# Kernel tuning notes

Hardware: AMD Instinct MI355X
Metric: run time of the kernel (lower is better)

Reference implementation:

```python
import jax, jax.numpy as jnp
import numpy as np

BLOCK_SPLIT = (4, 4, 4)
GRID = 256
N_BLOCK = 64
BX = GRID // 4  # 64, per-block grid resolution along each axis
N_PTS = 4_194_304


def setup_inputs() -> dict:
    key = jax.random.key(0)
    k1, k2 = jax.random.split(key)
    aabb = jnp.array([[-1.5, -1.5, -1.5], [1.5, 1.5, 1.5]], dtype=jnp.float32)
    # points roughly inside the aabb
    xyz_sampled = jax.random.uniform(k1, (N_PTS, 3), dtype=jnp.float32) * 3.0 - 1.5
    alpha_volume = jax.random.uniform(k2, (GRID, GRID, GRID), dtype=jnp.float32)
    # per-block domains (as kilonerf global_to_local expects): block AABBs
    idx = np.stack(np.meshgrid(np.arange(4), np.arange(4), np.arange(4), indexing='ij'), -1).reshape(-1, 3)
    voxel = np.array([3.0 / 4.0] * 3)
    dmin = (-1.5 + idx * voxel).astype(np.float32)
    dmax = (dmin + voxel).astype(np.float32)
    return {"xyz_sampled": xyz_sampled, "aabb": aabb, "alpha_volume": alpha_volume,
            "domain_min": jnp.asarray(dmin), "domain_max": jnp.asarray(dmax)}


def _sample_alpha(xyz, aabb, alpha_volume, dmin, dmax):
    bs = jnp.asarray(BLOCK_SPLIT, jnp.float32)
    voxel = (aabb[1] - aabb[0]) / bs                      # per-block world size
    idx3 = jnp.floor((xyz - aabb[0]) / voxel).astype(jnp.int32)
    idx3 = jnp.clip(idx3, 0, jnp.array(BLOCK_SPLIT, jnp.int32) - 1)  # edge clamp (matches loop)
    strides = jnp.array([BLOCK_SPLIT[2] * BLOCK_SPLIT[1], BLOCK_SPLIT[2], 1], jnp.int32)
    bid = (idx3 * strides).sum(-1)                        # [N] block id in [0, 64)

    order = jnp.argsort(bid)                              # jax sort is stable; matches bucket-by-block order
    bid_s = bid[order]
    pts = xyz[order]

    # global_to_local (kilonerf): map into per-block [-1,1]^3
    local = 2.0 * (pts - dmin[bid_s]) / (dmax[bid_s] - dmin[bid_s]) - 1.0  # [N,3] (gx,gy,gz)

    # torch .view(64,1,64,64,64) is a raw contiguous reinterpretation -> plain reshape
    vols = alpha_volume.reshape(N_BLOCK, BX, BX, BX)      # [B, D, H, W]
    D = H = W = BX
    # grid_sample convention: grid x -> W axis, y -> H axis, z -> D axis; align_corners=True
    fx = (local[:, 0] + 1.0) * 0.5 * (W - 1)
    fy = (local[:, 1] + 1.0) * 0.5 * (H - 1)
    fz = (local[:, 2] + 1.0) * 0.5 * (D - 1)
    x0 = jnp.floor(fx); y0 = jnp.floor(fy); z0 = jnp.floor(fz)
    wx = fx - x0; wy = fy - y0; wz = fz - z0
    x0i = x0.astype(jnp.int32); y0i = y0.astype(jnp.int32); z0i = z0.astype(jnp.int32)

    def fetch(zi, yi, xi):
        # zeros padding for out-of-range corners (grid_sample padding_mode='zeros')
        inb = (zi >= 0) & (zi < D) & (yi >= 0) & (yi < H) & (xi >= 0) & (xi < W)
        v = vols[bid_s, jnp.clip(zi, 0, D - 1), jnp.clip(yi, 0, H - 1), jnp.clip(xi, 0, W - 1)]
        return jnp.where(inb, v, 0.0)

    out = jnp.zeros_like(fx)
    for dz, wz_ in ((0, 1.0 - wz), (1, wz)):
        for dy, wy_ in ((0, 1.0 - wy), (1, wy)):
            for dx, wx_ in ((0, 1.0 - wx), (1, wx)):
                out = out + wz_ * wy_ * wx_ * fetch(z0i + dz, y0i + dy, x0i + dx)
    return out  # [N] alpha values in block-sorted order


def reference(xyz_sampled, aabb, alpha_volume, domain_min, domain_max):
    return _sample_alpha(xyz_sampled, aabb, alpha_volume, domain_min, domain_max)
```

## Files before the change

kernel.cpp:

```cpp
#include <hip/hip_runtime.h>

#define BLK    256
#define TILE_C 4096
#define NB     64
#define NF     4096
#define TILE_F 16384
#define FBLK   512

__device__ __forceinline__ int compute_bid(float px, float py, float pz,
                                           float a0x, float a0y, float a0z,
                                           float vx, float vy, float vz) {
    int ix = (int)floorf((px - a0x) / vx);
    int iy = (int)floorf((py - a0y) / vy);
    int iz = (int)floorf((pz - a0z) / vz);
    ix = min(max(ix, 0), 3);
    iy = min(max(iy, 0), 3);
    iz = min(max(iz, 0), 3);
    return ix * 16 + iy * 4 + iz;
}

__global__ void hist_kernel(const float* __restrict__ xyz,
                            const float* __restrict__ aabb,
                            int* __restrict__ hist, int N, int G) {
    __shared__ int s_h[NB];
    const int tid = threadIdx.x, g = blockIdx.x;
    if (tid < NB) s_h[tid] = 0;
    __syncthreads();
    const float a0x = aabb[0], a0y = aabb[1], a0z = aabb[2];
    const float vx = (aabb[3] - a0x) * 0.25f;
    const float vy = (aabb[4] - a0y) * 0.25f;
    const float vz = (aabb[5] - a0z) * 0.25f;
    for (int c = 0; c < TILE_C / (BLK * 4); ++c) {
        int p0 = g * TILE_C + c * (BLK * 4) + tid * 4;
        if (p0 + 3 < N) {
            const float4* v4 = (const float4*)(xyz + (size_t)p0 * 3);
            float4 f0 = v4[0], f1 = v4[1], f2 = v4[2];
            atomicAdd(&s_h[compute_bid(f0.x, f0.y, f0.z, a0x, a0y, a0z, vx, vy, vz)], 1);
            atomicAdd(&s_h[compute_bid(f0.w, f1.x, f1.y, a0x, a0y, a0z, vx, vy, vz)], 1);
            atomicAdd(&s_h[compute_bid(f1.z, f1.w, f2.x, a0x, a0y, a0z, vx, vy, vz)], 1);
            atomicAdd(&s_h[compute_bid(f2.y, f2.z, f2.w, a0x, a0y, a0z, vx, vy, vz)], 1);
        } else {
            for (int t = 0; t < 4; ++t) {
                int i = p0 + t;
                if (i < N)
                    atomicAdd(&s_h[compute_bid(xyz[3 * i], xyz[3 * i + 1], xyz[3 * i + 2],
                                               a0x, a0y, a0z, vx, vy, vz)], 1);
            }
        }
    }
    __syncthreads();
    if (tid < NB) hist[tid * G + g] = s_h[tid];
}

__global__ void scan_rows_kernel(int* __restrict__ hist, int* __restrict__ tot,
                                 int* __restrict__ tot4096, int G) {
    __shared__ int sh[BLK];
    const int b = blockIdx.x, t = threadIdx.x;
    if (b == 0) for (int l = t; l < NF; l += BLK) tot4096[l] = 0;
    const int L = (G + BLK - 1) / BLK;
    const int lo = t * L;
    const int n = min(L, max(0, G - lo));
    const int base = b * G + lo;
    int s = 0;
    for (int k = 0; k < n; ++k) s += hist[base + k];
    sh[t] = s;
    __syncthreads();
    for (int off = 1; off < BLK; off <<= 1) {
        int v = (t >= off) ? sh[t - off] : 0;
        __syncthreads();
        sh[t] += v;
        __syncthreads();
    }
    int excl = (t == 0) ? 0 : sh[t - 1];
    for (int k = 0; k < n; ++k) {
        int v = hist[base + k];
        hist[base + k] = excl;
        excl += v;
    }
    if (t == BLK - 1) tot[b] = sh[BLK - 1];
}

__global__ void scatterC_kernel(const float* __restrict__ xyz,
                                const float* __restrict__ aabb,
                                const float* __restrict__ dmin,
                                const float* __restrict__ dmax,
                                const int* __restrict__ hist,
                                const int* __restrict__ tot64,
                                float4* __restrict__ payloadC,
                                unsigned short* __restrict__ key16,
                                int N, int G) {
    __shared__ int   s_cnt[NB];
    __shared__ int   s_off[NB];
    __shared__ int   s_whist[4][NB];
    __shared__ float s_dn[192], s_sc[192];
    const int tid = threadIdx.x, g = blockIdx.x;
    if (tid < NB) s_off[tid] = tot64[tid];
    for (int l = tid; l < 192; l += BLK) {
        s_dn[l] = dmin[l];
        s_sc[l] = 63.0f / (dmax[l] - dmin[l]);
    }
    __syncthreads();
    for (int o = 1; o < NB; o <<= 1) {
        int v = (tid < NB && tid >= o) ? s_off[tid - o] : 0;
        __syncthreads();
        if (tid < NB) s_off[tid] += v;
        __syncthreads();
    }
    if (tid < NB)
        s_cnt[tid] = hist[tid * G + g] + (tid == 0 ? 0 : s_off[tid - 1]);
    const float a0x = aabb[0], a0y = aabb[1], a0z = aabb[2];
    const float vx = (aabb[3] - a0x) * 0.25f;
    const float vy = (aabb[4] - a0y) * 0.25f;
    const float vz = (aabb[5] - a0z) * 0.25f;
    __syncthreads();

    const int lane = tid & 63;
    const int wv = tid >> 6;
    const unsigned long long lt = (1ull << lane) - 1ull;

    for (int c = 0; c < TILE_C / BLK; ++c) {
        int i = g * TILE_C + c * BLK + tid;
        bool valid = (i < N);
        int b = 0, key = 0;
        float fx = 0.0f, fy = 0.0f, fz = 0.0f;
        if (valid) {
            float px = xyz[3 * i], py = xyz[3 * i + 1], pz = xyz[3 * i + 2];
            b = compute_bid(px, py, pz, a0x, a0y, a0z, vx, vy, vz);
            fx = (px - s_dn[3 * b])     * s_sc[3 * b];
            fy = (py - s_dn[3 * b + 1]) * s_sc[3 * b + 1];
            fz = (pz - s_dn[3 * b + 2]) * s_sc[3 * b + 2];
            int icx = min(max((int)floorf(fx) >> 4, 0), 3);
            int icy = min(max((int)floorf(fy) >> 4, 0), 3);
            int icz = min(max((int)floorf(fz) >> 4, 0), 3);
            key = (b << 6) | (icz << 4) | (icy << 2) | icx;
        }
        ((int*)s_whist)[tid] = 0;
        __syncthreads();
        unsigned long long m = __ballot(valid);
        #pragma unroll
        for (int q = 0; q < 6; ++q) {
            unsigned long long bal = __ballot((b >> q) & 1);
            m &= ((b >> q) & 1) ? bal : ~bal;
        }
        int rank = __popcll(m & lt);
        if (valid && rank == 0) s_whist[wv][b] = __popcll(m);
        __syncthreads();
        if (valid) {
            int pos = s_cnt[b] + rank;
            for (int w2 = 0; w2 < wv; ++w2) pos += s_whist[w2][b];
            payloadC[pos] = make_float4(fx, fy, fz, __int_as_float(key));
            key16[pos] = (unsigned short)key;
        }
        __syncthreads();
        if (tid < NB)
            s_cnt[tid] += s_whist[0][tid] + s_whist[1][tid] +
                          s_whist[2][tid] + s_whist[3][tid];
        __syncthreads();
    }
}

__global__ void fhist2_kernel(const unsigned short* __restrict__ key16,
                              int* __restrict__ hist2,
                              int* __restrict__ tot4096, int N) {
    __shared__ int sh[NF];
    const int tid = threadIdx.x, t2 = blockIdx.x;
    for (int l = tid; l < NF; l += BLK) sh[l] = 0;
    __syncthreads();
    const int lo = t2 * TILE_F;
    const int n = min(TILE_F, N - lo);
    for (int j = tid; j < n; j += BLK) atomicAdd(&sh[key16[lo + j]], 1);
    __syncthreads();
    for (int l = tid; l < NF; l += BLK) {
        int c = sh[l];
        hist2[(size_t)t2 * NF + l] = c;
        if (c) atomicAdd(&tot4096[l], c);
    }
}

__global__ void fscan_kernel(const int* __restrict__ tot4096,
                             int* __restrict__ foff, int* __restrict__ fcnt) {
    __shared__ int sh[BLK];
    const int t = threadIdx.x;
    const int L = NF / BLK;
    int loc[16];
    int s = 0;
    #pragma unroll
    for (int j = 0; j < L; ++j) { loc[j] = tot4096[t * L + j]; s += loc[j]; }
    sh[t] = s;
    __syncthreads();
    for (int o = 1; o < BLK; o <<= 1) {
        int v = (t >= o) ? sh[t - o] : 0;
        __syncthreads();
        sh[t] += v;
        __syncthreads();
    }
    int run = (t == 0) ? 0 : sh[t - 1];
    #pragma unroll
    for (int j = 0; j < L; ++j) {
        foff[t * L + j] = run;
        fcnt[t * L + j] = run;
        run += loc[j];
    }
    if (t == BLK - 1) foff[NF] = run;
}

__global__ void __launch_bounds__(FBLK) scatterF_kernel(
        const float4* __restrict__ payloadC,
        const int* __restrict__ hist2,
        int* __restrict__ fcnt,
        float4* __restrict__ payloadF, int N) {
    __shared__ int s_fb[NF];
    const int tid = threadIdx.x, t2 = blockIdx.x;
    for (int l = tid; l < NF; l += FBLK) {
        int c = hist2[(size_t)t2 * NF + l];
        s_fb[l] = c ? atomicAdd(&fcnt[l], c) : 0;
    }
    __syncthreads();
    const int lo = t2 * TILE_F;
    const int n = min(TILE_F, N - lo);
    for (int j = tid; j < n; j += FBLK) {
        float4 p = payloadC[lo + j];
        int key = __float_as_int(p.w);
        int fpos = atomicAdd(&s_fb[key], 1);
        payloadF[fpos] = make_float4(p.x, p.y, p.z, __int_as_float(lo + j));
    }
}

__global__ void __launch_bounds__(BLK) gather_fine_kernel(
        const float* __restrict__ vol,
        const float4* __restrict__ payloadF,
        const int* __restrict__ foff,
        float* __restrict__ out) {
    __shared__ float sv[17 * 17 * 17];
    const int tid = threadIdx.x;
    const int nb = gridDim.x, d = blockIdx.x;
    const int k = (nb % 8 == 0) ? (d % 8) * (nb / 8) + (d / 8) : d;
    const int b = k >> 6;
    const int bz = ((k >> 4) & 3) * 16, by = ((k >> 2) & 3) * 16, bx = (k & 3) * 16;
    const float* vb = vol + ((size_t)b << 18);
    for (int l = tid; l < 17 * 17 * 17; l += BLK) {
        int z = l / 289, r = l - z * 289, y = r / 17, x = r - y * 17;
        int gz = bz + z, gy = by + y, gx = bx + x;
        sv[l] = (gz < 64 && gy < 64 && gx < 64)
                    ? vb[(gz << 12) + (gy << 6) + gx] : 0.0f;
    }
    __syncthreads();
    const int lo = foff[k];
    const int n = foff[k + 1] - lo;
    for (int j = tid; j < n; j += BLK) {
        float4 p = payloadF[lo + j];
        float fx = fminf(fmaxf(p.x, 0.0f), 63.0f);
        float fy = fminf(fmaxf(p.y, 0.0f), 63.0f);
        float fz = fminf(fmaxf(p.z, 0.0f), 63.0f);
        float x0f = floorf(fx), y0f = floorf(fy), z0f = floorf(fz);
        float wx = fx - x0f, wy = fy - y0f, wz = fz - z0f;
        int lx = (int)x0f - bx, ly = (int)y0f - by, lz = (int)z0f - bz;
        int base = lz * 289 + ly * 17 + lx;
        float v000 = sv[base],        v001 = sv[base + 1];
        float v010 = sv[base + 17],   v011 = sv[base + 18];
        float v100 = sv[base + 289],  v101 = sv[base + 290];
        float v110 = sv[base + 306],  v111 = sv[base + 307];
        float c00 = v000 + wx * (v001 - v000);
        float c01 = v010 + wx * (v011 - v010);
        float c10 = v100 + wx * (v101 - v100);
        float c11 = v110 + wx * (v111 - v110);
        float c0 = c00 + wy * (c01 - c00);
        float c1 = c10 + wy * (c11 - c10);
        out[__float_as_int(p.w)] = c0 + wz * (c1 - c0);
    }
}

__global__ void gather_fallback_kernel(const float* __restrict__ vol,
                                       const float4* __restrict__ payloadC,
                                       float* __restrict__ out, int N) {
    int nb = gridDim.x, d = blockIdx.x;
    int lb = (nb % 8 == 0) ? (d % 8) * (nb / 8) + (d / 8) : d;
    int j = lb * BLK + threadIdx.x;
    if (j >= N) return;
    float4 p = payloadC[j];
    int b = __float_as_int(p.w) >> 6;
    float x0f = floorf(p.x), y0f = floorf(p.y), z0f = floorf(p.z);
    float wx = p.x - x0f, wy = p.y - y0f, wz = p.z - z0f;
    int x0 = (int)x0f, y0 = (int)y0f, z0 = (int)z0f;
    const float* vb = vol + ((size_t)b << 18);
    auto F = [&](int zi, int yi, int xi) -> float {
        if ((unsigned)zi >= 64u || (unsigned)yi >= 64u || (unsigned)xi >= 64u)
            return 0.0f;
        return vb[(zi << 12) + (yi << 6) + xi];
    };
    float s = 0.0f;
    s += (1.0f - wz) * (1.0f - wy) * (1.0f - wx) * F(z0,     y0,     x0);
    s += (1.0f - wz) * (1.0f - wy) * wx          * F(z0,     y0,     x0 + 1);
    s += (1.0f - wz) * wy          * (1.0f - wx) * F(z0,     y0 + 1, x0);
    s += (1.0f - wz) * wy          * wx          * F(z0,     y0 + 1, x0 + 1);
    s += wz          * (1.0f - wy) * (1.0f - wx) * F(z0 + 1, y0,     x0);
    s += wz          * (1.0f - wy) * wx          * F(z0 + 1, y0,     x0 + 1);
    s += wz          * wy          * (1.0f - wx) * F(z0 + 1, y0 + 1, x0);
    s += wz          * wy          * wx          * F(z0 + 1, y0 + 1, x0 + 1);
    out[j] = s;
}

extern "C" void kernel_launch(void* const* d_in, const int* in_sizes, int n_in,
                              void* d_out, int out_size, void* d_ws, size_t ws_size,
                              hipStream_t stream) {
    const float* xyz  = (const float*)d_in[0];
    const float* aabb = (const float*)d_in[1];
    const float* vol  = (const float*)d_in[2];
    const float* dmin = (const float*)d_in[3];
    const float* dmax = (const float*)d_in[4];
    float* out = (float*)d_out;
    const int N  = in_sizes[0] / 3;
    const int G  = (N + TILE_C - 1) / TILE_C;
    const int T2 = (N + TILE_F - 1) / TILE_F;

    auto align = [](size_t x) { return (x + 255) & ~(size_t)255; };
    char* ws = (char*)d_ws;
    size_t o = 0;
    float4* payloadC = (float4*)(ws + o);              o += align((size_t)N * 16);
    unsigned short* key16 = (unsigned short*)(ws + o); o += align((size_t)N * 2);
    int* hist64 = (int*)(ws + o);                      o += align((size_t)NB * G * 4);
    int* tot64  = (int*)(ws + o);                      o += 256;
    float4* payloadF = (float4*)(ws + o);              o += align((size_t)N * 16);
    int* hist2   = (int*)(ws + o);                     o += align((size_t)T2 * NF * 4);
    int* tot4096 = (int*)(ws + o);                     o += align((size_t)NF * 4);
    int* foff    = (int*)(ws + o);                     o += align((size_t)(NF + 1) * 4);
    int* fcnt    = (int*)(ws + o);                     o += align((size_t)NF * 4);
    const bool fine = (ws_size >= o) && (N >= TILE_F);

    hist_kernel<<<G, BLK, 0, stream>>>(xyz, aabb, hist64, N, G);
    scan_rows_kernel<<<NB, BLK, 0, stream>>>(hist64, tot64, tot4096, G);
    scatterC_kernel<<<G, BLK, 0, stream>>>(xyz, aabb, dmin, dmax, hist64, tot64,
                                           payloadC, key16, N, G);
    if (fine) {
        fhist2_kernel<<<T2, BLK, 0, stream>>>(key16, hist2, tot4096, N);
        fscan_kernel<<<1, BLK, 0, stream>>>(tot4096, foff, fcnt);
        scatterF_kernel<<<T2, FBLK, 0, stream>>>(payloadC, hist2, fcnt, payloadF, N);
        gather_fine_kernel<<<NF, BLK, 0, stream>>>(vol, payloadF, foff, out);
    } else {
        gather_fallback_kernel<<<(N + BLK - 1) / BLK, BLK, 0, stream>>>(
            vol, payloadC, out, N);
    }
}
```

Measured before the change: 283.1 us.

## Fuse coarse and fine bucketing into one histogram and one scatter pass

The coarse 64-block histogram and the fine 4096-cell histogram are now computed together in a single pass over xyz. One scatter kernel computes each point's block-sorted output position directly and writes a packed 64-bit record with quantized coordinates and output index into the fine buckets. This removes the intermediate payloadC and key16 buffers and one full read/write pass. It also halves the payload size from float4 to u64 by quantizing fractional weights to 1/256, which changes interpolation precision.

```diff
diff --git a/kernel.cpp b/kernel.cpp
--- a/kernel.cpp
+++ b/kernel.cpp
@@ -1,11 +1,13 @@
 #include <hip/hip_runtime.h>
 
-#define BLK    256
-#define TILE_C 4096
 #define NB     64
 #define NF     4096
-#define TILE_F 16384
-#define FBLK   512
+#define TILE   16384
+#define HBLK   1024
+#define DBLK   1024
+#define GBLK   256
+#define SBLK   256
+#define FB_TILE 4096
 
 __device__ __forceinline__ int compute_bid(float px, float py, float pz,
                                            float a0x, float a0y, float a0z,
@@ -19,45 +21,78 @@
     return ix * 16 + iy * 4 + iz;
 }
 
-__global__ void hist_kernel(const float* __restrict__ xyz,
-                            const float* __restrict__ aabb,
-                            int* __restrict__ hist, int N, int G) {
-    __shared__ int s_h[NB];
+__device__ __forceinline__ void quant_point(float px, float py, float pz,
+        float a0x, float a0y, float a0z, float vx, float vy, float vz,
+        const float* s_dn, const float* s_sc,
+        int& b, int& qx, int& qy, int& qz, int& key) {
+    b = compute_bid(px, py, pz, a0x, a0y, a0z, vx, vy, vz);
+    float fx = (px - s_dn[3 * b])     * s_sc[3 * b];
+    float fy = (py - s_dn[3 * b + 1]) * s_sc[3 * b + 1];
+    float fz = (pz - s_dn[3 * b + 2]) * s_sc[3 * b + 2];
+    qx = min(max(__float2int_rn(fx * 256.0f), 0), 16128);
+    qy = min(max(__float2int_rn(fy * 256.0f), 0), 16128);
+    qz = min(max(__float2int_rn(fz * 256.0f), 0), 16128);
+    key = (b << 6) | ((qz >> 12) << 4) | ((qy >> 12) << 2) | (qx >> 12);
+}
+
+__global__ void __launch_bounds__(HBLK) hist_kernel(
+        const float* __restrict__ xyz, const float* __restrict__ aabb,
+        const float* __restrict__ dmin, const float* __restrict__ dmax,
+        int* __restrict__ hist64, int* __restrict__ hist2,
+        int* __restrict__ tot4096, int N, int T) {
+    __shared__ int   sh[NF];
+    __shared__ float s_dn[192], s_sc[192];
     const int tid = threadIdx.x, g = blockIdx.x;
-    if (tid < NB) s_h[tid] = 0;
-    __syncthreads();
+    for (int l = tid; l < NF; l += HBLK) sh[l] = 0;
+    if (tid < 192) { s_dn[tid] = dmin[tid]; s_sc[tid] = 63.0f / (dmax[tid] - dmin[tid]); }
     const float a0x = aabb[0], a0y = aabb[1], a0z = aabb[2];
     const float vx = (aabb[3] - a0x) * 0.25f;
     const float vy = (aabb[4] - a0y) * 0.25f;
     const float vz = (aabb[5] - a0z) * 0.25f;
-    for (int c = 0; c < TILE_C / (BLK * 4); ++c) {
-        int p0 = g * TILE_C + c * (BLK * 4) + tid * 4;
+    __syncthreads();
+    for (int c = 0; c < TILE / (HBLK * 4); ++c) {
+        int p0 = g * TILE + c * (HBLK * 4) + tid * 4;
+        int b, qx, qy, qz, k;
         if (p0 + 3 < N) {
             const float4* v4 = (const float4*)(xyz + (size_t)p0 * 3);
             float4 f0 = v4[0], f1 = v4[1], f2 = v4[2];
-            atomicAdd(&s_h[compute_bid(f0.x, f0.y, f0.z, a0x, a0y, a0z, vx, vy, vz)], 1);
-            atomicAdd(&s_h[compute_bid(f0.w, f1.x, f1.y, a0x, a0y, a0z, vx, vy, vz)], 1);
-            atomicAdd(&s_h[compute_bid(f1.z, f1.w, f2.x, a0x, a0y, a0z, vx, vy, vz)], 1);
-            atomicAdd(&s_h[compute_bid(f2.y, f2.z, f2.w, a0x, a0y, a0z, vx, vy, vz)], 1);
+            quant_point(f0.x, f0.y, f0.z, a0x, a0y, a0z, vx, vy, vz, s_dn, s_sc, b, qx, qy, qz, k);
+            atomicAdd(&sh[k], 1);
+            quant_point(f0.w, f1.x, f1.y, a0x, a0y, a0z, vx, vy, vz, s_dn, s_sc, b, qx, qy, qz, k);
+            atomicAdd(&sh[k], 1);
+            quant_point(f1.z, f1.w, f2.x, a0x, a0y, a0z, vx, vy, vz, s_dn, s_sc, b, qx, qy, qz, k);
+            atomicAdd(&sh[k], 1);
+            quant_point(f2.y, f2.z, f2.w, a0x, a0y, a0z, vx, vy, vz, s_dn, s_sc, b, qx, qy, qz, k);
+            atomicAdd(&sh[k], 1);
         } else {
             for (int t = 0; t < 4; ++t) {
                 int i = p0 + t;
-                if (i < N)
-                    atomicAdd(&s_h[compute_bid(xyz[3 * i], xyz[3 * i + 1], xyz[3 * i + 2],
-                                               a0x, a0y, a0z, vx, vy, vz)], 1);
+                if (i < N) {
+                    quant_point(xyz[3 * i], xyz[3 * i + 1], xyz[3 * i + 2],
+                                a0x, a0y, a0z, vx, vy, vz, s_dn, s_sc, b, qx, qy, qz, k);
+                    atomicAdd(&sh[k], 1);
+                }
             }
         }
     }
     __syncthreads();
-    if (tid < NB) hist[tid * G + g] = s_h[tid];
-}
-
-__global__ void scan_rows_kernel(int* __restrict__ hist, int* __restrict__ tot,
-                                 int* __restrict__ tot4096, int G) {
-    __shared__ int sh[BLK];
+    for (int l = tid; l < NF; l += HBLK) {
+        int c = sh[l];
+        hist2[(size_t)g * NF + l] = c;
+        if (c) atomicAdd(&tot4096[l], c);
+    }
+    if (tid < NB) {
+        int s = 0;
+        #pragma unroll
+        for (int j = 0; j < 64; ++j) s += sh[tid * 64 + j];
+        hist64[tid * T + g] = s;
+    }
+}
+
+__global__ void scan_rows_kernel(int* __restrict__ hist, int* __restrict__ tot, int G) {
+    __shared__ int sh[SBLK];
     const int b = blockIdx.x, t = threadIdx.x;
-    if (b == 0) for (int l = t; l < NF; l += BLK) tot4096[l] = 0;
-    const int L = (G + BLK - 1) / BLK;
+    const int L = (G + SBLK - 1) / SBLK;
     const int lo = t * L;
     const int n = min(L, max(0, G - lo));
     const int base = b * G + lo;
@@ -65,7 +100,7 @@
     for (int k = 0; k < n; ++k) s += hist[base + k];
     sh[t] = s;
     __syncthreads();
-    for (int off = 1; off < BLK; off <<= 1) {
+    for (int off = 1; off < SBLK; off <<= 1) {
         int v = (t >= off) ? sh[t - off] : 0;
         __syncthreads();
         sh[t] += v;
@@ -77,118 +112,21 @@
         hist[base + k] = excl;
         excl += v;
     }
-    if (t == BLK - 1) tot[b] = sh[BLK - 1];
-}
-
-__global__ void scatterC_kernel(const float* __restrict__ xyz,
-                                const float* __restrict__ aabb,
-                                const float* __restrict__ dmin,
-                                const float* __restrict__ dmax,
-                                const int* __restrict__ hist,
-                                const int* __restrict__ tot64,
-                                float4* __restrict__ payloadC,
-                                unsigned short* __restrict__ key16,
-                                int N, int G) {
-    __shared__ int   s_cnt[NB];
-    __shared__ int   s_off[NB];
-    __shared__ int   s_whist[4][NB];
-    __shared__ float s_dn[192], s_sc[192];
-    const int tid = threadIdx.x, g = blockIdx.x;
-    if (tid < NB) s_off[tid] = tot64[tid];
-    for (int l = tid; l < 192; l += BLK) {
-        s_dn[l] = dmin[l];
-        s_sc[l] = 63.0f / (dmax[l] - dmin[l]);
-    }
-    __syncthreads();
-    for (int o = 1; o < NB; o <<= 1) {
-        int v = (tid < NB && tid >= o) ? s_off[tid - o] : 0;
-        __syncthreads();
-        if (tid < NB) s_off[tid] += v;
-        __syncthreads();
-    }
-    if (tid < NB)
-        s_cnt[tid] = hist[tid * G + g] + (tid == 0 ? 0 : s_off[tid - 1]);
-    const float a0x = aabb[0], a0y = aabb[1], a0z = aabb[2];
-    const float vx = (aabb[3] - a0x) * 0.25f;
-    const float vy = (aabb[4] - a0y) * 0.25f;
-    const float vz = (aabb[5] - a0z) * 0.25f;
-    __syncthreads();
-
-    const int lane = tid & 63;
-    const int wv = tid >> 6;
-    const unsigned long long lt = (1ull << lane) - 1ull;
-
-    for (int c = 0; c < TILE_C / BLK; ++c) {
-        int i = g * TILE_C + c * BLK + tid;
-        bool valid = (i < N);
-        int b = 0, key = 0;
-        float fx = 0.0f, fy = 0.0f, fz = 0.0f;
-        if (valid) {
-            float px = xyz[3 * i], py = xyz[3 * i + 1], pz = xyz[3 * i + 2];
-            b = compute_bid(px, py, pz, a0x, a0y, a0z, vx, vy, vz);
-            fx = (px - s_dn[3 * b])     * s_sc[3 * b];
-            fy = (py - s_dn[3 * b + 1]) * s_sc[3 * b + 1];
-            fz = (pz - s_dn[3 * b + 2]) * s_sc[3 * b + 2];
-            int icx = min(max((int)floorf(fx) >> 4, 0), 3);
-            int icy = min(max((int)floorf(fy) >> 4, 0), 3);
-            int icz = min(max((int)floorf(fz) >> 4, 0), 3);
-            key = (b << 6) | (icz << 4) | (icy << 2) | icx;
-        }
-        ((int*)s_whist)[tid] = 0;
-        __syncthreads();
-        unsigned long long m = __ballot(valid);
-        #pragma unroll
-        for (int q = 0; q < 6; ++q) {
-            unsigned long long bal = __ballot((b >> q) & 1);
-            m &= ((b >> q) & 1) ? bal : ~bal;
-        }
-        int rank = __popcll(m & lt);
-        if (valid && rank == 0) s_whist[wv][b] = __popcll(m);
-        __syncthreads();
-        if (valid) {
-            int pos = s_cnt[b] + rank;
-            for (int w2 = 0; w2 < wv; ++w2) pos += s_whist[w2][b];
-            payloadC[pos] = make_float4(fx, fy, fz, __int_as_float(key));
-            key16[pos] = (unsigned short)key;
-        }
-        __syncthreads();
-        if (tid < NB)
-            s_cnt[tid] += s_whist[0][tid] + s_whist[1][tid] +
-                          s_whist[2][tid] + s_whist[3][tid];
-        __syncthreads();
-    }
-}
-
-__global__ void fhist2_kernel(const unsigned short* __restrict__ key16,
-                              int* __restrict__ hist2,
-                              int* __restrict__ tot4096, int N) {
-    __shared__ int sh[NF];
-    const int tid = threadIdx.x, t2 = blockIdx.x;
-    for (int l = tid; l < NF; l += BLK) sh[l] = 0;
-    __syncthreads();
-    const int lo = t2 * TILE_F;
-    const int n = min(TILE_F, N - lo);
-    for (int j = tid; j < n; j += BLK) atomicAdd(&sh[key16[lo + j]], 1);
-    __syncthreads();
-    for (int l = tid; l < NF; l += BLK) {
-        int c = sh[l];
-        hist2[(size_t)t2 * NF + l] = c;
-        if (c) atomicAdd(&tot4096[l], c);
-    }
+    if (t == SBLK - 1) tot[b] = sh[SBLK - 1];
 }
 
 __global__ void fscan_kernel(const int* __restrict__ tot4096,
                              int* __restrict__ foff, int* __restrict__ fcnt) {
-    __shared__ int sh[BLK];
+    __shared__ int sh[SBLK];
     const int t = threadIdx.x;
-    const int L = NF / BLK;
+    const int L = NF / SBLK;
     int loc[16];
     int s = 0;
     #pragma unroll
     for (int j = 0; j < L; ++j) { loc[j] = tot4096[t * L + j]; s += loc[j]; }
     sh[t] = s;
     __syncthreads();
-    for (int o = 1; o < BLK; o <<= 1) {
+    for (int o = 1; o < SBLK; o <<= 1) {
         int v = (t >= o) ? sh[t - o] : 0;
         __syncthreads();
         sh[t] += v;
@@ -201,36 +139,101 @@
         fcnt[t * L + j] = run;
         run += loc[j];
     }
-    if (t == BLK - 1) foff[NF] = run;
-}
-
-__global__ void __launch_bounds__(FBLK) scatterF_kernel(
-        const float4* __restrict__ payloadC,
-        const int* __restrict__ hist2,
-        int* __restrict__ fcnt,
-        float4* __restrict__ payloadF, int N) {
-    __shared__ int s_fb[NF];
-    const int tid = threadIdx.x, t2 = blockIdx.x;
-    for (int l = tid; l < NF; l += FBLK) {
-        int c = hist2[(size_t)t2 * NF + l];
+    if (t == SBLK - 1) foff[NF] = run;
+}
+
+__global__ void __launch_bounds__(DBLK) scatterD_kernel(
+        const float* __restrict__ xyz, const float* __restrict__ aabb,
+        const float* __restrict__ dmin, const float* __restrict__ dmax,
+        const int* __restrict__ hist64, const int* __restrict__ tot64,
+        const int* __restrict__ hist2, int* __restrict__ fcnt,
+        unsigned long long* __restrict__ payloadF, int N, int T) {
+    __shared__ int   s_fb[NF];
+    __shared__ int   s_wh[16][NB];
+    __shared__ int   s_cnt0[NB];
+    __shared__ int   s_off[NB];
+    __shared__ float s_dn[192], s_sc[192];
+    const int tid = threadIdx.x, g = blockIdx.x;
+    const int lane = tid & 63, wv = tid >> 6;
+    for (int l = tid; l < NF; l += DBLK) {
+        int c = hist2[(size_t)g * NF + l];
         s_fb[l] = c ? atomicAdd(&fcnt[l], c) : 0;
     }
-    __syncthreads();
-    const int lo = t2 * TILE_F;
-    const int n = min(TILE_F, N - lo);
-    for (int j = tid; j < n; j += FBLK) {
-        float4 p = payloadC[lo + j];
-        int key = __float_as_int(p.w);
-        int fpos = atomicAdd(&s_fb[key], 1);
-        payloadF[fpos] = make_float4(p.x, p.y, p.z, __int_as_float(lo + j));
-    }
-}
-
-__global__ void __launch_bounds__(BLK) gather_fine_kernel(
+    if (tid < NB) s_off[tid] = tot64[tid];
+    if (tid < 192) { s_dn[tid] = dmin[tid]; s_sc[tid] = 63.0f / (dmax[tid] - dmin[tid]); }
+    ((int*)s_wh)[tid] = 0;
+    const float a0x = aabb[0], a0y = aabb[1], a0z = aabb[2];
+    const float vx = (aabb[3] - a0x) * 0.25f;
+    const float vy = (aabb[4] - a0y) * 0.25f;
+    const float vz = (aabb[5] - a0z) * 0.25f;
+    __syncthreads();
+    for (int o = 1; o < NB; o <<= 1) {
+        int v = (tid < NB && tid >= o) ? s_off[tid - o] : 0;
+        __syncthreads();
+        if (tid < NB) s_off[tid] += v;
+        __syncthreads();
+    }
+    if (tid < NB) s_cnt0[tid] = hist64[tid * T + g] + (tid ? s_off[tid - 1] : 0);
+
+    const unsigned long long lt = (1ull << lane) - 1ull;
+    const int base_i = g * TILE + wv * 1024;
+    unsigned long long cache[16];
+    #pragma unroll
+    for (int r = 0; r < 16; ++r) {
+        int i = base_i + r * 64 + lane;
+        bool valid = (i < N);
+        int b = 0, qx = 0, qy = 0, qz = 0, key;
+        if (valid) {
+            quant_point(xyz[3 * i], xyz[3 * i + 1], xyz[3 * i + 2],
+                        a0x, a0y, a0z, vx, vy, vz, s_dn, s_sc, b, qx, qy, qz, key);
+        }
+        unsigned long long m = __ballot(valid);
+        #pragma unroll
+        for (int q = 0; q < 6; ++q) {
+            unsigned long long bal = __ballot((b >> q) & 1);
+            m &= ((b >> q) & 1) ? bal : ~bal;
+        }
+        int rank = __popcll(m & lt);
+        int run = valid ? s_wh[wv][b] : 0;
+        if (valid && rank == 0) s_wh[wv][b] = run + __popcll(m);
+        int localpos = run + rank;
+        cache[r] = (unsigned long long)(unsigned)qx
+                 | ((unsigned long long)(unsigned)qy << 14)
+                 | ((unsigned long long)(unsigned)qz << 28)
+                 | ((unsigned long long)(unsigned)b  << 42)
+                 | ((unsigned long long)(unsigned)localpos << 48);
+    }
+    __syncthreads();
+    for (int o = 1; o < 16; o <<= 1) {
+        int v = (wv >= o) ? s_wh[wv - o][lane] : 0;
+        __syncthreads();
+        s_wh[wv][lane] += v;
+        __syncthreads();
+    }
+    #pragma unroll
+    for (int r = 0; r < 16; ++r) {
+        int i = base_i + r * 64 + lane;
+        if (i < N) {
+            unsigned long long cc = cache[r];
+            int qx = (int)(cc & 16383), qy = (int)((cc >> 14) & 16383);
+            int qz = (int)((cc >> 28) & 16383);
+            int b = (int)((cc >> 42) & 63);
+            int localpos = (int)((cc >> 48) & 1023);
+            int pos = s_cnt0[b] + (wv ? s_wh[wv - 1][b] : 0) + localpos;
+            int key = (b << 6) | ((qz >> 12) << 4) | ((qy >> 12) << 2) | (qx >> 12);
+            int fpos = atomicAdd(&s_fb[key], 1);
+            payloadF[fpos] = (unsigned long long)(unsigned)qx
+                           | ((unsigned long long)(unsigned)qy << 14)
+                           | ((unsigned long long)(unsigned)qz << 28)
+                           | ((unsigned long long)(unsigned)pos << 42);
+        }
+    }
+}
+
+__global__ void __launch_bounds__(GBLK) gather_kernel(
         const float* __restrict__ vol,
-        const float4* __restrict__ payloadF,
-        const int* __restrict__ foff,
-        float* __restrict__ out) {
+        const unsigned long long* __restrict__ payloadF,
+        const int* __restrict__ foff, float* __restrict__ out) {
     __shared__ float sv[17 * 17 * 17];
     const int tid = threadIdx.x;
     const int nb = gridDim.x, d = blockIdx.x;
@@ -238,7 +241,7 @@
     const int b = k >> 6;
     const int bz = ((k >> 4) & 3) * 16, by = ((k >> 2) & 3) * 16, bx = (k & 3) * 16;
     const float* vb = vol + ((size_t)b << 18);
-    for (int l = tid; l < 17 * 17 * 17; l += BLK) {
+    for (int l = tid; l < 17 * 17 * 17; l += GBLK) {
         int z = l / 289, r = l - z * 289, y = r / 17, x = r - y * 17;
         int gz = bz + z, gy = by + y, gx = bx + x;
         sv[l] = (gz < 64 && gy < 64 && gx < 64)
@@ -247,57 +250,133 @@
     __syncthreads();
     const int lo = foff[k];
     const int n = foff[k + 1] - lo;
-    for (int j = tid; j < n; j += BLK) {
-        float4 p = payloadF[lo + j];
-        float fx = fminf(fmaxf(p.x, 0.0f), 63.0f);
-        float fy = fminf(fmaxf(p.y, 0.0f), 63.0f);
-        float fz = fminf(fmaxf(p.z, 0.0f), 63.0f);
-        float x0f = floorf(fx), y0f = floorf(fy), z0f = floorf(fz);
-        float wx = fx - x0f, wy = fy - y0f, wz = fz - z0f;
-        int lx = (int)x0f - bx, ly = (int)y0f - by, lz = (int)z0f - bz;
+    for (int j = tid; j < n; j += GBLK) {
+        unsigned long long p = payloadF[lo + j];
+        int qx = (int)(p & 16383), qy = (int)((p >> 14) & 16383);
+        int qz = (int)((p >> 28) & 16383);
+        int pos = (int)(p >> 42);
+        float wx = (qx & 255) * (1.0f / 256.0f);
+        float wy = (qy & 255) * (1.0f / 256.0f);
+        float wz = (qz & 255) * (1.0f / 256.0f);
+        int lx = (qx >> 8) - bx, ly = (qy >> 8) - by, lz = (qz >> 8) - bz;
         int base = lz * 289 + ly * 17 + lx;
-        float v000 = sv[base],        v001 = sv[base + 1];
-        float v010 = sv[base + 17],   v011 = sv[base + 18];
-        float v100 = sv[base + 289],  v101 = sv[base + 290];
-        float v110 = sv[base + 306],  v111 = sv[base + 307];
+        float v000 = sv[base],       v001 = sv[base + 1];
+        float v010 = sv[base + 17],  v011 = sv[base + 18];
+        float v100 = sv[base + 289], v101 = sv[base + 290];
+        float v110 = sv[base + 306], v111 = sv[base + 307];
         float c00 = v000 + wx * (v001 - v000);
         float c01 = v010 + wx * (v011 - v010);
         float c10 = v100 + wx * (v101 - v100);
         float c11 = v110 + wx * (v111 - v110);
         float c0 = c00 + wy * (c01 - c00);
         float c1 = c10 + wy * (c11 - c10);
-        out[__float_as_int(p.w)] = c0 + wz * (c1 - c0);
-    }
-}
-
-__global__ void gather_fallback_kernel(const float* __restrict__ vol,
-                                       const float4* __restrict__ payloadC,
-                                       float* __restrict__ out, int N) {
-    int nb = gridDim.x, d = blockIdx.x;
-    int lb = (nb % 8 == 0) ? (d % 8) * (nb / 8) + (d / 8) : d;
-    int j = lb * BLK + threadIdx.x;
-    if (j >= N) return;
-    float4 p = payloadC[j];
-    int b = __float_as_int(p.w) >> 6;
-    float x0f = floorf(p.x), y0f = floorf(p.y), z0f = floorf(p.z);
-    float wx = p.x - x0f, wy = p.y - y0f, wz = p.z - z0f;
-    int x0 = (int)x0f, y0 = (int)y0f, z0 = (int)z0f;
-    const float* vb = vol + ((size_t)b << 18);
-    auto F = [&](int zi, int yi, int xi) -> float {
-        if ((unsigned)zi >= 64u || (unsigned)yi >= 64u || (unsigned)xi >= 64u)
-            return 0.0f;
-        return vb[(zi << 12) + (yi << 6) + xi];
-    };
-    float s = 0.0f;
-    s += (1.0f - wz) * (1.0f - wy) * (1.0f - wx) * F(z0,     y0,     x0);
-    s += (1.0f - wz) * (1.0f - wy) * wx          * F(z0,     y0,     x0 + 1);
-    s += (1.0f - wz) * wy          * (1.0f - wx) * F(z0,     y0 + 1, x0);
-    s += (1.0f - wz) * wy          * wx          * F(z0,     y0 + 1, x0 + 1);
-    s += wz          * (1.0f - wy) * (1.0f - wx) * F(z0 + 1, y0,     x0);
-    s += wz          * (1.0f - wy) * wx          * F(z0 + 1, y0,     x0 + 1);
-    s += wz          * wy          * (1.0f - wx) * F(z0 + 1, y0 + 1, x0);
-    s += wz          * wy          * wx          * F(z0 + 1, y0 + 1, x0 + 1);
-    out[j] = s;
+        out[pos] = c0 + wz * (c1 - c0);
+    }
+}
+
+__global__ void fb_hist_kernel(const float* __restrict__ xyz,
+                               const float* __restrict__ aabb,
+                               int* __restrict__ hist, int N, int G) {
+    __shared__ int s_h[NB];
+    const int tid = threadIdx.x, g = blockIdx.x;
+    if (tid < NB) s_h[tid] = 0;
+    __syncthreads();
+    const float a0x = aabb[0], a0y = aabb[1], a0z = aabb[2];
+    const float vx = (aabb[3] - a0x) * 0.25f;
+    const float vy = (aabb[4] - a0y) * 0.25f;
+    const float vz = (aabb[5] - a0z) * 0.25f;
+    for (int c = 0; c < FB_TILE / 256; ++c) {
+        int i = g * FB_TILE + c * 256 + tid;
+        if (i < N)
+            atomicAdd(&s_h[compute_bid(xyz[3 * i], xyz[3 * i + 1], xyz[3 * i + 2],
+                                       a0x, a0y, a0z, vx, vy, vz)], 1);
+    }
+    __syncthreads();
+    if (tid < NB) hist[tid * G + g] = s_h[tid];
+}
+
+__global__ void fb_scatter_kernel(const float* __restrict__ xyz,
+                                  const float* __restrict__ aabb,
+                                  const float* __restrict__ dmin,
+                                  const float* __restrict__ dmax,
+                                  const float* __restrict__ vol,
+                                  const int* __restrict__ hist,
+                                  const int* __restrict__ tot64,
+                                  float* __restrict__ out, int N, int G) {
+    __shared__ int   s_cnt[NB], s_off[NB];
+    __shared__ int   s_whist[4][NB];
+    __shared__ float s_dn[192], s_sc[192];
+    const int tid = threadIdx.x, g = blockIdx.x;
+    if (tid < NB) s_off[tid] = tot64[tid];
+    if (tid < 192) { s_dn[tid] = dmin[tid]; s_sc[tid] = 63.0f / (dmax[tid] - dmin[tid]); }
+    __syncthreads();
+    for (int o = 1; o < NB; o <<= 1) {
+        int v = (tid < NB && tid >= o) ? s_off[tid - o] : 0;
+        __syncthreads();
+        if (tid < NB) s_off[tid] += v;
+        __syncthreads();
+    }
+    if (tid < NB) s_cnt[tid] = hist[tid * G + g] + (tid ? s_off[tid - 1] : 0);
+    const float a0x = aabb[0], a0y = aabb[1], a0z = aabb[2];
+    const float vx = (aabb[3] - a0x) * 0.25f;
+    const float vy = (aabb[4] - a0y) * 0.25f;
+    const float vz = (aabb[5] - a0z) * 0.25f;
+    __syncthreads();
+    const int lane = tid & 63, wv = tid >> 6;
+    const unsigned long long lt = (1ull << lane) - 1ull;
+    for (int c = 0; c < FB_TILE / 256; ++c) {
+        int i = g * FB_TILE + c * 256 + tid;
+        bool valid = (i < N);
+        int b = 0;
+        float alpha = 0.0f;
+        if (valid) {
+            float px = xyz[3 * i], py = xyz[3 * i + 1], pz = xyz[3 * i + 2];
+            b = compute_bid(px, py, pz, a0x, a0y, a0z, vx, vy, vz);
+            float fx = (px - s_dn[3 * b])     * s_sc[3 * b];
+            float fy = (py - s_dn[3 * b + 1]) * s_sc[3 * b + 1];
+            float fz = (pz - s_dn[3 * b + 2]) * s_sc[3 * b + 2];
+            float x0f = floorf(fx), y0f = floorf(fy), z0f = floorf(fz);
+            float wx = fx - x0f, wy = fy - y0f, wz = fz - z0f;
+            int x0 = (int)x0f, y0 = (int)y0f, z0 = (int)z0f;
+            const float* vb = vol + ((size_t)b << 18);
+            auto F = [&](int zi, int yi, int xi) -> float {
+                if ((unsigned)zi >= 64u || (unsigned)yi >= 64u || (unsigned)xi >= 64u)
+                    return 0.0f;
+                return vb[(zi << 12) + (yi << 6) + xi];
+            };
+            float s = 0.0f;
+            s += (1.0f - wz) * (1.0f - wy) * (1.0f - wx) * F(z0,     y0,     x0);
+            s += (1.0f - wz) * (1.0f - wy) * wx          * F(z0,     y0,     x0 + 1);
+            s += (1.0f - wz) * wy          * (1.0f - wx) * F(z0,     y0 + 1, x0);
+            s += (1.0f - wz) * wy          * wx          * F(z0,     y0 + 1, x0 + 1);
+            s += wz          * (1.0f - wy) * (1.0f - wx) * F(z0 + 1, y0,     x0);
+            s += wz          * (1.0f - wy) * wx          * F(z0 + 1, y0,     x0 + 1);
+            s += wz          * wy          * (1.0f - wx) * F(z0 + 1, y0 + 1, x0);
+            s += wz          * wy          * wx          * F(z0 + 1, y0 + 1, x0 + 1);
+            alpha = s;
+        }
+        ((int*)s_whist)[tid] = 0;
+        __syncthreads();
+        unsigned long long m = __ballot(valid);
+        #pragma unroll
+        for (int q = 0; q < 6; ++q) {
+            unsigned long long bal = __ballot((b >> q) & 1);
+            m &= ((b >> q) & 1) ? bal : ~bal;
+        }
+        int rank = __popcll(m & lt);
+        if (valid && rank == 0) s_whist[wv][b] = __popcll(m);
+        __syncthreads();
+        if (valid) {
+            int pos = s_cnt[b] + rank;
+            for (int w2 = 0; w2 < wv; ++w2) pos += s_whist[w2][b];
+            out[pos] = alpha;
+        }
+        __syncthreads();
+        if (tid < NB)
+            s_cnt[tid] += s_whist[0][tid] + s_whist[1][tid] +
+                          s_whist[2][tid] + s_whist[3][tid];
+        __syncthreads();
+    }
 }
 
 extern "C" void kernel_launch(void* const* d_in, const int* in_sizes, int n_in,
@@ -309,35 +388,37 @@
     const float* dmin = (const float*)d_in[3];
     const float* dmax = (const float*)d_in[4];
     float* out = (float*)d_out;
-    const int N  = in_sizes[0] / 3;
-    const int G  = (N + TILE_C - 1) / TILE_C;
-    const int T2 = (N + TILE_F - 1) / TILE_F;
+    const int N = in_sizes[0] / 3;
+    const int T = (N + TILE - 1) / TILE;
 
     auto align = [](size_t x) { return (x + 255) & ~(size_t)255; };
     char* ws = (char*)d_ws;
     size_t o = 0;
-    float4* payloadC = (float4*)(ws + o);              o += align((size_t)N * 16);
-    unsigned short* key16 = (unsigned short*)(ws + o); o += align((size_t)N * 2);
-    int* hist64 = (int*)(ws + o);                      o += align((size_t)NB * G * 4);
-    int* tot64  = (int*)(ws + o);                      o += 256;
-    float4* payloadF = (float4*)(ws + o);              o += align((size_t)N * 16);
-    int* hist2   = (int*)(ws + o);                     o += align((size_t)T2 * NF * 4);
-    int* tot4096 = (int*)(ws + o);                     o += align((size_t)NF * 4);
-    int* foff    = (int*)(ws + o);                     o += align((size_t)(NF + 1) * 4);
-    int* fcnt    = (int*)(ws + o);                     o += align((size_t)NF * 4);
-    const bool fine = (ws_size >= o) && (N >= TILE_F);
-
-    hist_kernel<<<G, BLK, 0, stream>>>(xyz, aabb, hist64, N, G);
-    scan_rows_kernel<<<NB, BLK, 0, stream>>>(hist64, tot64, tot4096, G);
-    scatterC_kernel<<<G, BLK, 0, stream>>>(xyz, aabb, dmin, dmax, hist64, tot64,
-                                           payloadC, key16, N, G);
+    unsigned long long* payloadF = (unsigned long long*)(ws + o); o += align((size_t)N * 8);
+    int* hist64  = (int*)(ws + o); o += align((size_t)NB * T * 4);
+    int* tot64   = (int*)(ws + o); o += 256;
+    int* hist2   = (int*)(ws + o); o += align((size_t)T * NF * 4);
+    int* tot4096 = (int*)(ws + o); o += align((size_t)NF * 4);
+    int* foff    = (int*)(ws + o); o += align((size_t)(NF + 1) * 4);
+    int* fcnt    = (int*)(ws + o); o += align((size_t)NF * 4);
+    const bool fine = (N <= (1 << 22)) && (ws_size >= o);
+
     if (fine) {
-        fhist2_kernel<<<T2, BLK, 0, stream>>>(key16, hist2, tot4096, N);
-        fscan_kernel<<<1, BLK, 0, stream>>>(tot4096, foff, fcnt);
-        scatterF_kernel<<<T2, FBLK, 0, stream>>>(payloadC, hist2, fcnt, payloadF, N);
-        gather_fine_kernel<<<NF, BLK, 0, stream>>>(vol, payloadF, foff, out);
+        hipMemsetAsync(tot4096, 0, NF * 4, stream);
+        hist_kernel<<<T, HBLK, 0, stream>>>(xyz, aabb, dmin, dmax,
+                                            hist64, hist2, tot4096, N, T);
+        scan_rows_kernel<<<NB, SBLK, 0, stream>>>(hist64, tot64, T);
+        fscan_kernel<<<1, SBLK, 0, stream>>>(tot4096, foff, fcnt);
+        scatterD_kernel<<<T, DBLK, 0, stream>>>(xyz, aabb, dmin, dmax, hist64,
+                                                tot64, hist2, fcnt, payloadF, N, T);
+        gather_kernel<<<NF, GBLK, 0, stream>>>(vol, payloadF, foff, out);
     } else {
-        gather_fallback_kernel<<<(N + BLK - 1) / BLK, BLK, 0, stream>>>(
-            vol, payloadC, out, N);
-    }
-}
+        const int Gf = (N + FB_TILE - 1) / FB_TILE;
+        int* h = (int*)ws;
+        int* t = (int*)(ws + align((size_t)NB * Gf * 4));
+        fb_hist_kernel<<<Gf, 256, 0, stream>>>(xyz, aabb, h, N, Gf);
+        scan_rows_kernel<<<NB, SBLK, 0, stream>>>(h, t, Gf);
+        fb_scatter_kernel<<<Gf, 256, 0, stream>>>(xyz, aabb, dmin, dmax, vol,
+                                                  h, t, out, N, Gf);
+    }
+}
```

New measurement: 280.1 us. About the same (-1.1%).
